# Performance work log

Measured on AMD Instinct MI355X. Metric: run time of the kernel, lower is better.

The kernel has to match this reference:

```python
import jax, jax.numpy as jnp
import numpy as np

B, L, D, H = 4, 2048, 1024, 16
HD = D // H
EPS_LN = 1e-12
EPS_Z = 1e-6


def _rope_tables(seq_len, d_model, base=10000.0):
    k_max = d_model // 2
    theta = 1.0 / (base ** (np.arange(k_max, dtype=np.float32) / k_max))
    ang = np.arange(seq_len, dtype=np.float32)[:, None] * theta[None, :]  # [L, D/2]
    return jnp.asarray(np.cos(ang)), jnp.asarray(np.sin(ang))


def _apply_rope(x, cos, sin):
    # x: [B, L, D]; complex rotation on (even, odd) pairs of last dim
    xr, xi = x[..., 0::2], x[..., 1::2]          # [B, L, D/2]
    or_ = xr * cos - xi * sin
    oi = xr * sin + xi * cos
    return jnp.stack([or_, oi], axis=-1).reshape(x.shape)


def _layernorm(x, g, b):
    mu = jnp.mean(x, axis=-1, keepdims=True)
    var = jnp.mean(jnp.square(x - mu), axis=-1, keepdims=True)
    return (x - mu) * jax.lax.rsqrt(var + EPS_LN) * g + b


def _heads(t):
    # [B, L, D] -> [B, H, L, HD]
    return t.reshape(B, L, H, HD).transpose(0, 2, 1, 3)


def _attn(x, W_qk, b_qk, conv_w, conv_b, cos, sin):
    # x: [B, L, D] (output of in_proj)
    qk = x @ W_qk + b_qk                                  # [B, L, 2D]
    q = jax.nn.elu(qk[..., :D]) + 1.0
    k = jax.nn.elu(qk[..., D:]) + 1.0
    v = x
    q_rope = _heads(_apply_rope(q, cos, sin))             # [B, H, L, HD]
    k_rope = _heads(_apply_rope(k, cos, sin))
    qh, kh, vh = _heads(q), _heads(k), _heads(v)
    # normalizer: 1 / (q . mean_L(k))
    k_mean = jnp.mean(kh, axis=2)                          # [B, H, HD]
    z = 1.0 / (jnp.einsum('bhld,bhd->bhl', qh, k_mean) + EPS_Z)  # [B, H, L]
    # kv accumulation (global, scaled by 1/L via two L^-0.5 factors)
    kv = jnp.einsum('bhld,bhle->bhde', k_rope, vh) / L     # [B, H, HD, HD]
    out = jnp.einsum('bhld,bhde->bhle', q_rope, kv) * z[..., None]  # [B,H,L,HD]
    out = out.transpose(0, 2, 1, 3).reshape(B, L, D)
    # depthwise causal conv + SiLU on v (left pad k-1=3, keep length L)
    v_t = v.transpose(0, 2, 1)                             # [B, D, L]
    conv = jax.lax.conv_general_dilated(
        v_t, conv_w, window_strides=(1,), padding=[(3, 0)],
        dimension_numbers=('NCH', 'OIH', 'NCH'), feature_group_count=D)
    conv = jax.nn.silu(conv + conv_b[:, None])             # [B, D, L]
    return out + conv.transpose(0, 2, 1)


def setup_inputs() -> dict:
    key = jax.random.key(0)
    ks = jax.random.split(key, 12)
    s = 0.02
    return {
        'x': jax.random.normal(ks[0], (B, L, D), jnp.float32),
        'ln1_g': jnp.ones((D,), jnp.float32), 'ln1_b': jnp.zeros((D,), jnp.float32),
        'ln2_g': jnp.ones((D,), jnp.float32), 'ln2_b': jnp.zeros((D,), jnp.float32),
        'W_act': jax.random.normal(ks[1], (D, D), jnp.float32) * s,
        'b_act': jnp.zeros((D,), jnp.float32),
        'W_in': jax.random.normal(ks[2], (D, D), jnp.float32) * s,
        'b_in': jnp.zeros((D,), jnp.float32),
        'W_qk': jax.random.normal(ks[3], (D, 2 * D), jnp.float32) * s,
        'b_qk': jnp.zeros((2 * D,), jnp.float32),
        'conv_w': jax.random.normal(ks[4], (D, 1, 4), jnp.float32) * 0.25,
        'conv_b': jnp.zeros((D,), jnp.float32),
        'W_out': jax.random.normal(ks[5], (D, D), jnp.float32) * s,
        'b_out': jnp.zeros((D,), jnp.float32),
        'W1': jax.random.normal(ks[6], (D, 4 * D), jnp.float32) * s,
        'b1': jnp.zeros((4 * D,), jnp.float32),
        'W2': jax.random.normal(ks[7], (4 * D, D), jnp.float32) * s,
        'b2': jnp.zeros((D,), jnp.float32),
    }


def reference(x, ln1_g, ln1_b, ln2_g, ln2_b, W_act, b_act, W_in, b_in,
              W_qk, b_qk, conv_w, conv_b, W_out, b_out, W1, b1, W2, b2):
    cos, sin = _rope_tables(L, D)
    shortcut = x
    h = _layernorm(x, ln1_g, ln1_b)
    act_res = jax.nn.silu(h @ W_act + b_act)
    h = h @ W_in + b_in
    h = _attn(h, W_qk, b_qk, conv_w, conv_b, cos, sin)
    h = (h * act_res) @ W_out + b_out
    x = shortcut + h
    m = _layernorm(x, ln2_g, ln2_b)
    m = jax.nn.gelu(m @ W1 + b1, approximate=False) @ W2 + b2
    return x + m
```

## Files before the change

### kernel.cpp

```cpp
#include <hip/hip_runtime.h>
#include <math.h>

typedef unsigned short ushort_t;
typedef __attribute__((ext_vector_type(4))) float f32x4;
typedef __attribute__((ext_vector_type(8))) __bf16 bf16x8;
typedef __attribute__((ext_vector_type(8))) unsigned short u16x8;
typedef __attribute__((ext_vector_type(4))) unsigned short u16x4;

#define DEV __device__ __forceinline__

#define CB 4
#define CL 2048
#define CD 1024
#define CM 8192

DEV float bf2f(ushort_t u) {
  unsigned int x = ((unsigned int)u) << 16;
  return __builtin_bit_cast(float, x);
}
DEV ushort_t f2bf(float f) {
  unsigned int u = __builtin_bit_cast(unsigned int, f);
  u += 0x7FFFu + ((u >> 16) & 1u);
  return (ushort_t)(u >> 16);
}
DEV void gload16(const void* g, void* l) {
  __builtin_amdgcn_global_load_lds((const __attribute__((address_space(1))) void*)g,
                                   (__attribute__((address_space(3))) void*)l, 16, 0, 0);
}
DEV bf16x8 frag64(const ushort_t* s, int row, int slog) {
  int sl = slog ^ (row & 7);
  return __builtin_bit_cast(bf16x8, *reinterpret_cast<const u16x8*>(s + row * 64 + sl * 8));
}

DEV void tr_tile(const float* __restrict__ src, ushort_t* __restrict__ dst, int R, int C, int bx,
                 int by, int t) {
  __shared__ float tile[32][33];
  int c0 = bx * 32, r0 = by * 32;
  int tx = t & 31, ty = t >> 5;
#pragma unroll
  for (int i = 0; i < 32; i += 8) tile[ty + i][tx] = src[(size_t)(r0 + ty + i) * C + c0 + tx];
  __syncthreads();
#pragma unroll
  for (int i = 0; i < 32; i += 8) dst[(size_t)(c0 + ty + i) * R + r0 + tx] = f2bf(tile[tx][ty + i]);
}

__global__ __launch_bounds__(256) void k_prep(const float* __restrict__ W_act,
                                              const float* __restrict__ W_in,
                                              const float* __restrict__ W_qk,
                                              const float* __restrict__ W_out,
                                              const float* __restrict__ W1,
                                              const float* __restrict__ W2,
                                              ushort_t* __restrict__ WabT,
                                              ushort_t* __restrict__ WqkT,
                                              ushort_t* __restrict__ WoutT,
                                              ushort_t* __restrict__ W1T,
                                              ushort_t* __restrict__ W2T,
                                              ushort_t* __restrict__ cosT,
                                              ushort_t* __restrict__ sinT) {
  int bid = blockIdx.x, t = threadIdx.x;
  if (bid < 4096) {
    int idx = bid * 256 + t;
    int l = idx >> 9, j = idx & 511;
    float theta = exp2f(-(float)j * (13.2877123795494f / 512.0f));
    float ang = (float)l * theta;
    float s, c;
    sincosf(ang, &s, &c);
    cosT[idx] = f2bf(c);
    sinT[idx] = f2bf(s);
  } else if (bid < 5120) {
    int lo = bid - 4096;
    tr_tile(W_act, WabT, 1024, 1024, lo & 31, lo >> 5, t);
  } else if (bid < 6144) {
    int lo = bid - 5120;
    tr_tile(W_in, WabT + (size_t)1024 * 1024, 1024, 1024, lo & 31, lo >> 5, t);
  } else if (bid < 8192) {
    int lo = bid - 6144;
    tr_tile(W_qk, WqkT, 1024, 2048, lo & 63, lo >> 6, t);
  } else if (bid < 9216) {
    int lo = bid - 8192;
    tr_tile(W_out, WoutT, 1024, 1024, lo & 31, lo >> 5, t);
  } else if (bid < 13312) {
    int lo = bid - 9216;
    tr_tile(W1, W1T, 1024, 4096, lo & 127, lo >> 7, t);
  } else {
    int lo = bid - 13312;
    tr_tile(W2, W2T, 4096, 1024, lo & 31, lo >> 5, t);
  }
}

__global__ __launch_bounds__(256) void k_layernorm(const float* __restrict__ x,
                                                   const float* __restrict__ g,
                                                   const float* __restrict__ b,
                                                   ushort_t* __restrict__ out) {
  int row = blockIdx.x, t = threadIdx.x;
  const float* xr = x + (size_t)row * CD;
  f32x4 v = ((const f32x4*)xr)[t];
  float s = v.x + v.y + v.z + v.w;
  float s2 = v.x * v.x + v.y * v.y + v.z * v.z + v.w * v.w;
#pragma unroll
  for (int off = 32; off >= 1; off >>= 1) {
    s += __shfl_xor(s, off);
    s2 += __shfl_xor(s2, off);
  }
  __shared__ float red[8];
  int lane = t & 63, w = t >> 6;
  if (lane == 0) { red[w] = s; red[w + 4] = s2; }
  __syncthreads();
  s = red[0] + red[1] + red[2] + red[3];
  s2 = red[4] + red[5] + red[6] + red[7];
  float mu = s * (1.0f / CD);
  float var = s2 * (1.0f / CD) - mu * mu;
  float rs = rsqrtf(var + 1e-12f);
  f32x4 gg = ((const f32x4*)g)[t];
  f32x4 bb = ((const f32x4*)b)[t];
  u16x4 o;
  o.x = f2bf((v.x - mu) * rs * gg.x + bb.x);
  o.y = f2bf((v.y - mu) * rs * gg.y + bb.y);
  o.z = f2bf((v.z - mu) * rs * gg.z + bb.z);
  o.w = f2bf((v.w - mu) * rs * gg.w + bb.w);
  ((u16x4*)(out + (size_t)row * CD))[t] = o;
}

enum { EP_AV = 0, EP_ELU1 = 1, EP_GELU = 2, EP_ADDX = 3 };

template <int EP>
__global__ __launch_bounds__(256, 4) void k_gemm(const ushort_t* __restrict__ A,
                                                 const ushort_t* __restrict__ Bt, int N, int K,
                                                 const float* __restrict__ bias,
                                                 const float* __restrict__ bias2,
                                                 const float* __restrict__ addf,
                                                 float* __restrict__ outf,
                                                 ushort_t* __restrict__ outb,
                                                 ushort_t* __restrict__ out2) {
  __shared__ __align__(16) ushort_t sA[128 * 64];
  __shared__ __align__(16) ushort_t sB[128 * 64];
  const int t = threadIdx.x;
  const int lane = t & 63;
  const int w = t >> 6;
  const int wr = w >> 1, wc = w & 1;
  const int m0 = blockIdx.y * 128, n0 = blockIdx.x * 128;

  f32x4 acc[4][4];
#pragma unroll
  for (int i = 0; i < 4; ++i)
#pragma unroll
    for (int j = 0; j < 4; ++j) acc[i][j] = f32x4{0.f, 0.f, 0.f, 0.f};

  for (int kt = 0; kt < K; kt += 64) {
#pragma unroll
    for (int i = 0; i < 4; ++i) {
      int c = t + i * 256;
      int row = c >> 3;
      int sl = (c & 7) ^ (row & 7);
      int ldsoff = (w * 64 + i * 256) * 8;
      gload16(A + (size_t)(m0 + row) * K + kt + sl * 8, sA + ldsoff);
      gload16(Bt + (size_t)(n0 + row) * K + kt + sl * 8, sB + ldsoff);
    }
    __syncthreads();
#pragma unroll
    for (int kk = 0; kk < 2; ++kk) {
      int slog = kk * 4 + (lane >> 4);
      bf16x8 af[4], bfr[4];
#pragma unroll
      for (int mi = 0; mi < 4; ++mi) af[mi] = frag64(sA, wr * 64 + mi * 16 + (lane & 15), slog);
#pragma unroll
      for (int ni = 0; ni < 4; ++ni) bfr[ni] = frag64(sB, wc * 64 + ni * 16 + (lane & 15), slog);
#pragma unroll
      for (int mi = 0; mi < 4; ++mi)
#pragma unroll
        for (int ni = 0; ni < 4; ++ni)
          acc[mi][ni] =
              __builtin_amdgcn_mfma_f32_16x16x32_bf16(af[mi], bfr[ni], acc[mi][ni], 0, 0, 0);
    }
    __syncthreads();
  }

#pragma unroll
  for (int mi = 0; mi < 4; ++mi) {
#pragma unroll
    for (int ni = 0; ni < 4; ++ni) {
      int col = n0 + wc * 64 + ni * 16 + (lane & 15);
#pragma unroll
      for (int r = 0; r < 4; ++r) {
        int row = m0 + wr * 64 + mi * 16 + (lane >> 4) * 4 + r;
        if constexpr (EP == EP_AV) {
          if (col < 1024) {
            float vv = acc[mi][ni][r] + bias[col];
            outb[(size_t)row * 1024 + col] = f2bf(vv / (1.f + expf(-vv)));
          } else {
            float vv = acc[mi][ni][r] + bias2[col - 1024];
            out2[(size_t)row * 1024 + (col - 1024)] = f2bf(vv);
          }
        } else if constexpr (EP == EP_ELU1) {
          float vv = acc[mi][ni][r] + bias[col];
          outb[(size_t)row * N + col] = f2bf(vv > 0.f ? vv + 1.f : expf(vv));
        } else if constexpr (EP == EP_GELU) {
          float vv = acc[mi][ni][r] + bias[col];
          outb[(size_t)row * N + col] = f2bf(0.5f * vv * (1.f + erff(vv * 0.70710678118654752f)));
        } else {
          size_t idx = (size_t)row * N + col;
          outf[idx] = addf[idx] + acc[mi][ni][r] + bias[col];
        }
      }
    }
  }
}

__global__ __launch_bounds__(256) void k_attn_reduce(const ushort_t* __restrict__ qk,
                                                     const ushort_t* __restrict__ vbf,
                                                     const ushort_t* __restrict__ cosT,
                                                     const ushort_t* __restrict__ sinT,
                                                     float* __restrict__ kvpart,
                                                     float* __restrict__ kmpart) {
  int bh = blockIdx.x >> 2, ls = blockIdx.x & 3;
  int b = bh >> 4, h = bh & 15;
  int t = threadIdx.x, lane = t & 63, w = t >> 6;

  __shared__ float kst[64][68];
  __shared__ __align__(16) ushort_t krT[64 * 64];
  __shared__ __align__(16) ushort_t vT[64 * 64];
  __shared__ float cst[64][32];
  __shared__ float snt[64][32];
  __shared__ float kmp[4][64];

  float kmacc = 0.f;
  f32x4 acc[4];
#pragma unroll
  for (int i = 0; i < 4; ++i) acc[i] = f32x4{0.f, 0.f, 0.f, 0.f};

  for (int c = ls * 8; c < ls * 8 + 8; ++c) {
    int l0 = c * 64;
    for (int idx = t; idx < 4096; idx += 256) {
      int l = idx >> 6, d = idx & 63;
      size_t grow = (size_t)(b * CL + l0 + l);
      float kvv = bf2f(qk[grow * 2048 + 1024 + h * 64 + d]);
      kst[l][d] = kvv;
      kmacc += kvv;
      ushort_t vv = vbf[grow * CD + h * 64 + d];
      int sl = (l >> 3) ^ (d & 7);
      vT[d * 64 + sl * 8 + (l & 7)] = vv;
    }
    for (int idx = t; idx < 2048; idx += 256) {
      int l = idx >> 5, j = idx & 31;
      size_t p = (size_t)(l0 + l) * 512 + h * 32 + j;
      cst[l][j] = bf2f(cosT[p]);
      snt[l][j] = bf2f(sinT[p]);
    }
    __syncthreads();
    for (int idx = t; idx < 4096; idx += 256) {
      int l = idx >> 6, d = idx & 63, j = d >> 1;
      float cc = cst[l][j], sn = snt[l][j];
      float kr = (d & 1) ? (kst[l][d - 1] * sn + kst[l][d] * cc)
                         : (kst[l][d] * cc - kst[l][d + 1] * sn);
      int sl = (l >> 3) ^ (d & 7);
      krT[d * 64 + sl * 8 + (l & 7)] = f2bf(kr);
    }
    __syncthreads();
#pragma unroll
    for (int kk = 0; kk < 2; ++kk) {
      int slog = kk * 4 + (lane >> 4);
      bf16x8 a = frag64(vT, w * 16 + (lane & 15), slog);
#pragma unroll
      for (int ni = 0; ni < 4; ++ni) {
        bf16x8 bb = frag64(krT, ni * 16 + (lane & 15), slog);
        acc[ni] = __builtin_amdgcn_mfma_f32_16x16x32_bf16(a, bb, acc[ni], 0, 0, 0);
      }
    }
    __syncthreads();
  }
  float* kp = kvpart + ((size_t)(bh * 4 + ls)) * 4096;
#pragma unroll
  for (int ni = 0; ni < 4; ++ni) {
    int d = ni * 16 + (lane & 15);
#pragma unroll
    for (int r = 0; r < 4; ++r) {
      int e = w * 16 + (lane >> 4) * 4 + r;
      kp[e * 64 + d] = acc[ni][r];
    }
  }
  kmp[t >> 6][t & 63] = kmacc;
  __syncthreads();
  if (t < 64) kmpart[(bh * 4 + ls) * 64 + t] = kmp[0][t] + kmp[1][t] + kmp[2][t] + kmp[3][t];
}

__global__ void k_kv_reduce(const float* __restrict__ kvpart, const float* __restrict__ kmpart,
                            ushort_t* __restrict__ kvT, float* __restrict__ kmean) {
  int gid = blockIdx.x * 256 + threadIdx.x;
  int bh = gid >> 12;
  int r = gid & 4095;
  float s = 0.f;
#pragma unroll
  for (int ls = 0; ls < 4; ++ls) s += kvpart[((size_t)(bh * 4 + ls)) * 4096 + r];
  kvT[gid] = f2bf(s);
  if (gid < 64 * 64) {
    int bh2 = gid >> 6, d = gid & 63;
    float m = 0.f;
#pragma unroll
    for (int ls = 0; ls < 4; ++ls) m += kmpart[(bh2 * 4 + ls) * 64 + d];
    kmean[gid] = m;
  }
}

__global__ __launch_bounds__(256) void k_attn_out(
    const ushort_t* __restrict__ qk, const ushort_t* __restrict__ kvT,
    const float* __restrict__ kmean, const ushort_t* __restrict__ cosT,
    const ushort_t* __restrict__ sinT, const ushort_t* __restrict__ vbf,
    const ushort_t* __restrict__ act, const float* __restrict__ convw,
    const float* __restrict__ convb, ushort_t* __restrict__ A4) {
  int bid = blockIdx.x;
  int bh = bid >> 5, lt = bid & 31;
  int b = bh >> 4, h = bh & 15;
  int l0 = lt * 64;
  int t = threadIdx.x, lane = t & 63, w = t >> 6;

  __shared__ float qst[64][68];
  __shared__ __align__(16) ushort_t qrT[64 * 64];
  __shared__ __align__(16) ushort_t kvs[64 * 64];
  __shared__ float cst[64][32];
  __shared__ float snt[64][32];
  __shared__ float kms[64];
  __shared__ float zrow[64];

  if (t < 64) kms[t] = kmean[bh * 64 + t];
  for (int idx = t; idx < 4096; idx += 256) {
    int l = idx >> 6, d = idx & 63;
    qst[l][d] = bf2f(qk[(size_t)(b * CL + l0 + l) * 2048 + h * 64 + d]);
    ushort_t kvv = kvT[(size_t)bh * 4096 + idx];
    int e = idx >> 6, dd = idx & 63;
    int sl = (dd >> 3) ^ (e & 7);
    kvs[e * 64 + sl * 8 + (dd & 7)] = kvv;
  }
  for (int idx = t; idx < 2048; idx += 256) {
    int l = idx >> 5, j = idx & 31;
    size_t p = (size_t)(l0 + l) * 512 + h * 32 + j;
    cst[l][j] = bf2f(cosT[p]);
    snt[l][j] = bf2f(sinT[p]);
  }
  __syncthreads();
  for (int idx = t; idx < 4096; idx += 256) {
    int l = idx >> 6, d = idx & 63, j = d >> 1;
    float cc = cst[l][j], sn = snt[l][j];
    float qr = (d & 1) ? (qst[l][d - 1] * sn + qst[l][d] * cc)
                       : (qst[l][d] * cc - qst[l][d + 1] * sn);
    int sl = (d >> 3) ^ (l & 7);
    qrT[l * 64 + sl * 8 + (d & 7)] = f2bf(qr);
  }
  if (t < 64) {
    float dot = 0.f;
#pragma unroll
    for (int d = 0; d < 64; ++d) dot += qst[t][d] * kms[d];
    zrow[t] = 1.0f / (dot * (1.0f / (float)CL) + 1e-6f);
  }
  __syncthreads();
  f32x4 acc[4];
#pragma unroll
  for (int i = 0; i < 4; ++i) acc[i] = f32x4{0.f, 0.f, 0.f, 0.f};
#pragma unroll
  for (int kk = 0; kk < 2; ++kk) {
    int slog = kk * 4 + (lane >> 4);
    bf16x8 a = frag64(qrT, w * 16 + (lane & 15), slog);
#pragma unroll
    for (int ni = 0; ni < 4; ++ni) {
      bf16x8 bb = frag64(kvs, ni * 16 + (lane & 15), slog);
      acc[ni] = __builtin_amdgcn_mfma_f32_16x16x32_bf16(a, bb, acc[ni], 0, 0, 0);
    }
  }
#pragma unroll
  for (int ni = 0; ni < 4; ++ni) {
    int e = ni * 16 + (lane & 15);
    int dcol = h * 64 + e;
#pragma unroll
    for (int r = 0; r < 4; ++r) {
      int l = w * 16 + (lane >> 4) * 4 + r;
      int lg = l0 + l;
      size_t row = (size_t)(b * CL + lg);
      float val = acc[ni][r] * zrow[l] * (1.0f / (float)CL);
      float cv = convb[dcol];
#pragma unroll
      for (int tt = 0; tt < 4; ++tt) {
        if (lg - 3 + tt >= 0) cv += bf2f(vbf[(row - 3 + tt) * CD + dcol]) * convw[dcol * 4 + tt];
      }
      cv = cv / (1.f + expf(-cv));
      float a4 = (val + cv) * bf2f(act[row * CD + dcol]);
      A4[row * CD + dcol] = f2bf(a4);
    }
  }
}

extern "C" void kernel_launch(void* const* d_in, const int* in_sizes, int n_in, void* d_out,
                              int out_size, void* d_ws, size_t ws_size, hipStream_t stream) {
  const float* x = (const float*)d_in[0];
  const float* ln1_g = (const float*)d_in[1];
  const float* ln1_b = (const float*)d_in[2];
  const float* ln2_g = (const float*)d_in[3];
  const float* ln2_b = (const float*)d_in[4];
  const float* W_act = (const float*)d_in[5];
  const float* b_act = (const float*)d_in[6];
  const float* W_in = (const float*)d_in[7];
  const float* b_in = (const float*)d_in[8];
  const float* W_qk = (const float*)d_in[9];
  const float* b_qk = (const float*)d_in[10];
  const float* conv_w = (const float*)d_in[11];
  const float* conv_b = (const float*)d_in[12];
  const float* W_out = (const float*)d_in[13];
  const float* b_out = (const float*)d_in[14];
  const float* W1 = (const float*)d_in[15];
  const float* b1 = (const float*)d_in[16];
  const float* W2 = (const float*)d_in[17];
  const float* b2 = (const float*)d_in[18];
  float* out = (float*)d_out;

  char* w = (char*)d_ws;
  const size_t MB = 1024 * 1024;
  ushort_t* cosT = (ushort_t*)(w + 0 * MB);
  ushort_t* sinT = (ushort_t*)(w + 2 * MB);
  ushort_t* WabT = (ushort_t*)(w + 4 * MB);
  ushort_t* WqkT = (ushort_t*)(w + 8 * MB);
  ushort_t* WoutT = (ushort_t*)(w + 12 * MB);
  ushort_t* kvTb = (ushort_t*)(w + 14 * MB);
  float* kmean = (float*)(w + 14 * MB + 512 * 1024);
  float* kmpart = (float*)(w + 14 * MB + 640 * 1024);
  ushort_t* mln = (ushort_t*)(w + 0 * MB);
  ushort_t* W1T = (ushort_t*)(w + 16 * MB);
  ushort_t* W2T = (ushort_t*)(w + 24 * MB);
  ushort_t* hln = (ushort_t*)(w + 32 * MB);
  ushort_t* qkb = (ushort_t*)(w + 48 * MB);
  ushort_t* actb = (ushort_t*)(w + 80 * MB);
  ushort_t* Gb = (ushort_t*)(w + 32 * MB);
  ushort_t* vb = (ushort_t*)(w + 96 * MB);
  ushort_t* A4 = (ushort_t*)(w + 112 * MB);
  float* kvpart = (float*)(w + 112 * MB);
  float* x2 = (float*)(w + 128 * MB);

  (void)in_sizes; (void)n_in; (void)out_size; (void)ws_size;

  k_prep<<<17408, 256, 0, stream>>>(W_act, W_in, W_qk, W_out, W1, W2, WabT, WqkT, WoutT, W1T, W2T,
                                    cosT, sinT);
  k_layernorm<<<CM, 256, 0, stream>>>(x, ln1_g, ln1_b, hln);
  k_gemm<EP_AV><<<dim3(16, 64), 256, 0, stream>>>(hln, WabT, 2048, 1024, b_act, b_in, nullptr,
                                                  nullptr, actb, vb);
  k_gemm<EP_ELU1><<<dim3(16, 64), 256, 0, stream>>>(vb, WqkT, 2048, 1024, b_qk, nullptr, nullptr,
                                                    nullptr, qkb, nullptr);
  k_attn_reduce<<<256, 256, 0, stream>>>(qkb, vb, cosT, sinT, kvpart, kmpart);
  k_kv_reduce<<<1024, 256, 0, stream>>>(kvpart, kmpart, kvTb, kmean);
  k_attn_out<<<2048, 256, 0, stream>>>(qkb, kvTb, kmean, cosT, sinT, vb, actb, conv_w, conv_b, A4);
  k_gemm<EP_ADDX><<<dim3(8, 64), 256, 0, stream>>>(A4, WoutT, 1024, 1024, b_out, nullptr, x, x2,
                                                   nullptr, nullptr);
  k_layernorm<<<CM, 256, 0, stream>>>(x2, ln2_g, ln2_b, mln);
  k_gemm<EP_GELU><<<dim3(32, 64), 256, 0, stream>>>(mln, W1T, 4096, 1024, b1, nullptr, nullptr,
                                                    nullptr, Gb, nullptr);
  k_gemm<EP_ADDX><<<dim3(8, 64), 256, 0, stream>>>(Gb, W2T, 1024, 4096, b2, nullptr, x2, out,
                                                   nullptr, nullptr);
}
```

Measured before the change: 470.7 us.

## Split-K the N=1024 GEMMs, fuse residual add into LayerNorm, remap block IDs

```diff
diff --git a/kernel.cpp b/kernel.cpp
--- a/kernel.cpp
+++ b/kernel.cpp
@@ -121,14 +121,64 @@
   ((u16x4*)(out + (size_t)row * CD))[t] = o;
 }
 
-enum { EP_AV = 0, EP_ELU1 = 1, EP_GELU = 2, EP_ADDX = 3 };
+__global__ __launch_bounds__(256) void k_addln(const float* __restrict__ x,
+                                               const float* __restrict__ bo,
+                                               const float* __restrict__ P,
+                                               const float* __restrict__ g,
+                                               const float* __restrict__ b,
+                                               float* __restrict__ x2,
+                                               ushort_t* __restrict__ mln) {
+  int row = blockIdx.x, t = threadIdx.x;
+  size_t base = (size_t)row * CD;
+  f32x4 v = ((const f32x4*)(x + base))[t];
+  v += ((const f32x4*)(P + base))[t];
+  v += ((const f32x4*)(P + (size_t)8388608 + base))[t];
+  v += ((const f32x4*)bo)[t];
+  ((f32x4*)(x2 + base))[t] = v;
+  float s = v.x + v.y + v.z + v.w;
+  float s2 = v.x * v.x + v.y * v.y + v.z * v.z + v.w * v.w;
+#pragma unroll
+  for (int off = 32; off >= 1; off >>= 1) {
+    s += __shfl_xor(s, off);
+    s2 += __shfl_xor(s2, off);
+  }
+  __shared__ float red[8];
+  int lane = t & 63, w = t >> 6;
+  if (lane == 0) { red[w] = s; red[w + 4] = s2; }
+  __syncthreads();
+  s = red[0] + red[1] + red[2] + red[3];
+  s2 = red[4] + red[5] + red[6] + red[7];
+  float mu = s * (1.0f / CD);
+  float var = s2 * (1.0f / CD) - mu * mu;
+  float rs = rsqrtf(var + 1e-12f);
+  f32x4 gg = ((const f32x4*)g)[t];
+  f32x4 bb = ((const f32x4*)b)[t];
+  u16x4 o;
+  o.x = f2bf((v.x - mu) * rs * gg.x + bb.x);
+  o.y = f2bf((v.y - mu) * rs * gg.y + bb.y);
+  o.z = f2bf((v.z - mu) * rs * gg.z + bb.z);
+  o.w = f2bf((v.w - mu) * rs * gg.w + bb.w);
+  ((u16x4*)(mln + base))[t] = o;
+}
+
+__global__ void k_final(const float* __restrict__ x2, const float* __restrict__ b2,
+                        const float* __restrict__ P, float* __restrict__ out) {
+  size_t i = (size_t)blockIdx.x * 256 + threadIdx.x;
+  f32x4 v = ((const f32x4*)x2)[i];
+  v += ((const f32x4*)P)[i];
+  v += ((const f32x4*)(P + 8388608))[i];
+  v += ((const f32x4*)b2)[(int)(i & 255)];
+  ((f32x4*)out)[i] = v;
+}
+
+enum { EP_AV = 0, EP_ELU1 = 1, EP_GELU = 2, EP_KS = 3 };
 
 template <int EP>
 __global__ __launch_bounds__(256, 4) void k_gemm(const ushort_t* __restrict__ A,
-                                                 const ushort_t* __restrict__ Bt, int N, int K,
+                                                 const ushort_t* __restrict__ Bt, int N, int lda,
+                                                 int ldb, int Klen, int nbx, int nks,
                                                  const float* __restrict__ bias,
                                                  const float* __restrict__ bias2,
-                                                 const float* __restrict__ addf,
                                                  float* __restrict__ outf,
                                                  ushort_t* __restrict__ outb,
                                                  ushort_t* __restrict__ out2) {
@@ -138,7 +188,17 @@
   const int lane = t & 63;
   const int w = t >> 6;
   const int wr = w >> 1, wc = w & 1;
-  const int m0 = blockIdx.y * 128, n0 = blockIdx.x * 128;
+  const int lr = lane & 15, lq = lane >> 4;
+
+  int bid = blockIdx.x;
+  int q = gridDim.x >> 3;
+  int wg = (bid & 7) * q + (bid >> 3);
+  int by = wg / (nbx * nks);
+  int rem = wg - by * (nbx * nks);
+  int bx = rem / nks;
+  int ks = rem - bx * nks;
+  const int m0 = by * 128, n0 = bx * 128;
+  const int koff = ks * Klen;
 
   f32x4 acc[4][4];
 #pragma unroll
@@ -146,25 +206,25 @@
 #pragma unroll
     for (int j = 0; j < 4; ++j) acc[i][j] = f32x4{0.f, 0.f, 0.f, 0.f};
 
-  for (int kt = 0; kt < K; kt += 64) {
+  for (int kt = 0; kt < Klen; kt += 64) {
 #pragma unroll
     for (int i = 0; i < 4; ++i) {
       int c = t + i * 256;
       int row = c >> 3;
       int sl = (c & 7) ^ (row & 7);
       int ldsoff = (w * 64 + i * 256) * 8;
-      gload16(A + (size_t)(m0 + row) * K + kt + sl * 8, sA + ldsoff);
-      gload16(Bt + (size_t)(n0 + row) * K + kt + sl * 8, sB + ldsoff);
+      gload16(A + (size_t)(m0 + row) * lda + koff + kt + sl * 8, sA + ldsoff);
+      gload16(Bt + (size_t)(n0 + row) * ldb + koff + kt + sl * 8, sB + ldsoff);
     }
     __syncthreads();
 #pragma unroll
     for (int kk = 0; kk < 2; ++kk) {
-      int slog = kk * 4 + (lane >> 4);
+      int slog = kk * 4 + lq;
       bf16x8 af[4], bfr[4];
 #pragma unroll
-      for (int mi = 0; mi < 4; ++mi) af[mi] = frag64(sA, wr * 64 + mi * 16 + (lane & 15), slog);
-#pragma unroll
-      for (int ni = 0; ni < 4; ++ni) bfr[ni] = frag64(sB, wc * 64 + ni * 16 + (lane & 15), slog);
+      for (int mi = 0; mi < 4; ++mi) af[mi] = frag64(sA, wr * 64 + mi * 16 + lr, slog);
+#pragma unroll
+      for (int ni = 0; ni < 4; ++ni) bfr[ni] = frag64(sB, wc * 64 + ni * 16 + lr, slog);
 #pragma unroll
       for (int mi = 0; mi < 4; ++mi)
 #pragma unroll
@@ -179,10 +239,10 @@
   for (int mi = 0; mi < 4; ++mi) {
 #pragma unroll
     for (int ni = 0; ni < 4; ++ni) {
-      int col = n0 + wc * 64 + ni * 16 + (lane & 15);
+      int col = n0 + wc * 64 + ni * 16 + lr;
 #pragma unroll
       for (int r = 0; r < 4; ++r) {
-        int row = m0 + wr * 64 + mi * 16 + (lane >> 4) * 4 + r;
+        int row = m0 + wr * 64 + mi * 16 + lq * 4 + r;
         if constexpr (EP == EP_AV) {
           if (col < 1024) {
             float vv = acc[mi][ni][r] + bias[col];
@@ -198,8 +258,7 @@
           float vv = acc[mi][ni][r] + bias[col];
           outb[(size_t)row * N + col] = f2bf(0.5f * vv * (1.f + erff(vv * 0.70710678118654752f)));
         } else {
-          size_t idx = (size_t)row * N + col;
-          outf[idx] = addf[idx] + acc[mi][ni][r] + bias[col];
+          outf[(size_t)ks * 8388608 + (size_t)row * N + col] = acc[mi][ni][r];
         }
       }
     }
@@ -430,25 +489,27 @@
   ushort_t* vb = (ushort_t*)(w + 96 * MB);
   ushort_t* A4 = (ushort_t*)(w + 112 * MB);
   float* kvpart = (float*)(w + 112 * MB);
-  float* x2 = (float*)(w + 128 * MB);
+  float* x2 = (float*)(w + 96 * MB);
+  float* PP = (float*)(w + 128 * MB);
 
   (void)in_sizes; (void)n_in; (void)out_size; (void)ws_size;
 
   k_prep<<<17408, 256, 0, stream>>>(W_act, W_in, W_qk, W_out, W1, W2, WabT, WqkT, WoutT, W1T, W2T,
                                     cosT, sinT);
   k_layernorm<<<CM, 256, 0, stream>>>(x, ln1_g, ln1_b, hln);
-  k_gemm<EP_AV><<<dim3(16, 64), 256, 0, stream>>>(hln, WabT, 2048, 1024, b_act, b_in, nullptr,
-                                                  nullptr, actb, vb);
-  k_gemm<EP_ELU1><<<dim3(16, 64), 256, 0, stream>>>(vb, WqkT, 2048, 1024, b_qk, nullptr, nullptr,
-                                                    nullptr, qkb, nullptr);
+  k_gemm<EP_AV><<<1024, 256, 0, stream>>>(hln, WabT, 2048, 1024, 1024, 1024, 16, 1, b_act, b_in,
+                                          nullptr, actb, vb);
+  k_gemm<EP_ELU1><<<1024, 256, 0, stream>>>(vb, WqkT, 2048, 1024, 1024, 1024, 16, 1, b_qk, nullptr,
+                                            nullptr, qkb, nullptr);
   k_attn_reduce<<<256, 256, 0, stream>>>(qkb, vb, cosT, sinT, kvpart, kmpart);
   k_kv_reduce<<<1024, 256, 0, stream>>>(kvpart, kmpart, kvTb, kmean);
   k_attn_out<<<2048, 256, 0, stream>>>(qkb, kvTb, kmean, cosT, sinT, vb, actb, conv_w, conv_b, A4);
-  k_gemm<EP_ADDX><<<dim3(8, 64), 256, 0, stream>>>(A4, WoutT, 1024, 1024, b_out, nullptr, x, x2,
-                                                   nullptr, nullptr);
-  k_layernorm<<<CM, 256, 0, stream>>>(x2, ln2_g, ln2_b, mln);
-  k_gemm<EP_GELU><<<dim3(32, 64), 256, 0, stream>>>(mln, W1T, 4096, 1024, b1, nullptr, nullptr,
-                                                    nullptr, Gb, nullptr);
-  k_gemm<EP_ADDX><<<dim3(8, 64), 256, 0, stream>>>(Gb, W2T, 1024, 4096, b2, nullptr, x2, out,
-                                                   nullptr, nullptr);
-}
+  k_gemm<EP_KS><<<1024, 256, 0, stream>>>(A4, WoutT, 1024, 1024, 1024, 512, 8, 2, nullptr, nullptr,
+                                          PP, nullptr, nullptr);
+  k_addln<<<CM, 256, 0, stream>>>(x, b_out, PP, ln2_g, ln2_b, x2, mln);
+  k_gemm<EP_GELU><<<2048, 256, 0, stream>>>(mln, W1T, 4096, 1024, 1024, 1024, 32, 1, b1, nullptr,
+                                            nullptr, Gb, nullptr);
+  k_gemm<EP_KS><<<1024, 256, 0, stream>>>(Gb, W2T, 1024, 4096, 4096, 2048, 8, 2, nullptr, nullptr,
+                                          PP, nullptr, nullptr);
+  k_final<<<8192, 256, 0, stream>>>(x2, b2, PP, out);
+}
```

After: 513.5 us. 9.1% more time.

## Add pipelined 256x256 GEMM kernel for FFN up-projection with tanh GELU

Applied to the files above, without the earlier changes.

```diff
diff --git a/kernel.cpp b/kernel.cpp
--- a/kernel.cpp
+++ b/kernel.cpp
@@ -30,6 +30,12 @@
 DEV bf16x8 frag64(const ushort_t* s, int row, int slog) {
   int sl = slog ^ (row & 7);
   return __builtin_bit_cast(bf16x8, *reinterpret_cast<const u16x8*>(s + row * 64 + sl * 8));
+}
+DEV float gelu_f(float x) {
+  float u = 0.7978845608f * (x + 0.044715f * x * x * x);
+  float e = __expf(2.0f * u);
+  float th = 1.0f - 2.0f / (e + 1.0f);
+  return 0.5f * x * (1.0f + th);
 }
 
 DEV void tr_tile(const float* __restrict__ src, ushort_t* __restrict__ dst, int R, int C, int bx,
@@ -64,7 +70,7 @@
     float theta = exp2f(-(float)j * (13.2877123795494f / 512.0f));
     float ang = (float)l * theta;
     float s, c;
-    sincosf(ang, &s, &c);
+    __sincosf(ang, &s, &c);
     cosT[idx] = f2bf(c);
     sinT[idx] = f2bf(s);
   } else if (bid < 5120) {
@@ -121,7 +127,7 @@
   ((u16x4*)(out + (size_t)row * CD))[t] = o;
 }
 
-enum { EP_AV = 0, EP_ELU1 = 1, EP_GELU = 2, EP_ADDX = 3 };
+enum { EP_AV = 0, EP_ELU1 = 1, EP_ADDX = 3 };
 
 template <int EP>
 __global__ __launch_bounds__(256, 4) void k_gemm(const ushort_t* __restrict__ A,
@@ -138,6 +144,7 @@
   const int lane = t & 63;
   const int w = t >> 6;
   const int wr = w >> 1, wc = w & 1;
+  const int lr = lane & 15, lq = lane >> 4;
   const int m0 = blockIdx.y * 128, n0 = blockIdx.x * 128;
 
   f32x4 acc[4][4];
@@ -159,12 +166,12 @@
     __syncthreads();
 #pragma unroll
     for (int kk = 0; kk < 2; ++kk) {
-      int slog = kk * 4 + (lane >> 4);
+      int slog = kk * 4 + lq;
       bf16x8 af[4], bfr[4];
 #pragma unroll
-      for (int mi = 0; mi < 4; ++mi) af[mi] = frag64(sA, wr * 64 + mi * 16 + (lane & 15), slog);
-#pragma unroll
-      for (int ni = 0; ni < 4; ++ni) bfr[ni] = frag64(sB, wc * 64 + ni * 16 + (lane & 15), slog);
+      for (int mi = 0; mi < 4; ++mi) af[mi] = frag64(sA, wr * 64 + mi * 16 + lr, slog);
+#pragma unroll
+      for (int ni = 0; ni < 4; ++ni) bfr[ni] = frag64(sB, wc * 64 + ni * 16 + lr, slog);
 #pragma unroll
       for (int mi = 0; mi < 4; ++mi)
 #pragma unroll
@@ -179,28 +186,143 @@
   for (int mi = 0; mi < 4; ++mi) {
 #pragma unroll
     for (int ni = 0; ni < 4; ++ni) {
-      int col = n0 + wc * 64 + ni * 16 + (lane & 15);
+      int col = n0 + wc * 64 + ni * 16 + lr;
 #pragma unroll
       for (int r = 0; r < 4; ++r) {
-        int row = m0 + wr * 64 + mi * 16 + (lane >> 4) * 4 + r;
+        int row = m0 + wr * 64 + mi * 16 + lq * 4 + r;
         if constexpr (EP == EP_AV) {
           if (col < 1024) {
             float vv = acc[mi][ni][r] + bias[col];
-            outb[(size_t)row * 1024 + col] = f2bf(vv / (1.f + expf(-vv)));
+            outb[(size_t)row * 1024 + col] = f2bf(vv / (1.f + __expf(-vv)));
           } else {
             float vv = acc[mi][ni][r] + bias2[col - 1024];
             out2[(size_t)row * 1024 + (col - 1024)] = f2bf(vv);
           }
         } else if constexpr (EP == EP_ELU1) {
           float vv = acc[mi][ni][r] + bias[col];
-          outb[(size_t)row * N + col] = f2bf(vv > 0.f ? vv + 1.f : expf(vv));
-        } else if constexpr (EP == EP_GELU) {
-          float vv = acc[mi][ni][r] + bias[col];
-          outb[(size_t)row * N + col] = f2bf(0.5f * vv * (1.f + erff(vv * 0.70710678118654752f)));
+          outb[(size_t)row * N + col] = f2bf(vv > 0.f ? vv + 1.f : __expf(vv));
         } else {
           size_t idx = (size_t)row * N + col;
           outf[idx] = addf[idx] + acc[mi][ni][r] + bias[col];
         }
+      }
+    }
+  }
+}
+
+#define STGA8(h_, kt_, b_)                                                              \
+  {                                                                                     \
+    gload16(pA0 + (size_t)(h_)*131072 + (kt_), smem + (b_)*32768 + (h_)*8192 + dof0);   \
+    gload16(pA1 + (size_t)(h_)*131072 + (kt_), smem + (b_)*32768 + (h_)*8192 + dof1);   \
+  }
+#define STGB8(h_, kt_, b_)                                                                  \
+  {                                                                                         \
+    gload16(pB0 + (size_t)(h_)*131072 + (kt_), smem + (b_)*32768 + 16384 + (h_)*8192 + dof0); \
+    gload16(pB1 + (size_t)(h_)*131072 + (kt_), smem + (b_)*32768 + 16384 + (h_)*8192 + dof1); \
+  }
+#define PHASE8(mh_, nh_, RA_, BF_, RB_)                                                     \
+  {                                                                                         \
+    if (RA_) {                                                                              \
+      _Pragma("unroll") for (int mi = 0; mi < 4; ++mi)                                      \
+          _Pragma("unroll") for (int kk = 0; kk < 2; ++kk)                                  \
+              af[mi][kk] = frag64(sA, wr * 128 + (mh_)*64 + mi * 16 + lr, kk * 4 + lq);     \
+    }                                                                                       \
+    if (RB_) {                                                                              \
+      _Pragma("unroll") for (int ni = 0; ni < 2; ++ni)                                      \
+          _Pragma("unroll") for (int kk = 0; kk < 2; ++kk)                                  \
+              BF_[ni][kk] = frag64(sB, wc * 64 + (nh_)*32 + ni * 16 + lr, kk * 4 + lq);     \
+    }                                                                                       \
+    __builtin_amdgcn_s_barrier();                                                           \
+    asm volatile("s_waitcnt lgkmcnt(0)" ::: "memory");                                      \
+    __builtin_amdgcn_sched_barrier(0);                                                      \
+    __builtin_amdgcn_s_setprio(1);                                                          \
+    _Pragma("unroll") for (int kk = 0; kk < 2; ++kk)                                        \
+        _Pragma("unroll") for (int mi = 0; mi < 4; ++mi)                                    \
+            _Pragma("unroll") for (int ni = 0; ni < 2; ++ni)                                \
+                acc[(mh_)*4 + mi][(nh_)*2 + ni] = __builtin_amdgcn_mfma_f32_16x16x32_bf16(  \
+                    af[mi][kk], BF_[ni][kk], acc[(mh_)*4 + mi][(nh_)*2 + ni], 0, 0, 0);     \
+    __builtin_amdgcn_s_setprio(0);                                                          \
+    __builtin_amdgcn_sched_barrier(0);                                                      \
+    __builtin_amdgcn_s_barrier();                                                           \
+  }
+
+__global__ __launch_bounds__(512, 1) void k_gemm8(const ushort_t* __restrict__ A,
+                                                  const ushort_t* __restrict__ Bt, int N, int lda,
+                                                  int ldb, int Klen, int nbx,
+                                                  const float* __restrict__ bias,
+                                                  ushort_t* __restrict__ outb) {
+  __shared__ __align__(16) ushort_t smem[2 * 32768];
+  const int t = threadIdx.x;
+  const int lane = t & 63, w = t >> 6;
+  const int wr = w >> 2, wc = w & 3;
+  const int lr = lane & 15, lq = lane >> 4;
+
+  int bid = blockIdx.x;
+  int by = bid / nbx, bx = bid - by * nbx;
+  const int m0 = by << 8, n0 = bx << 8;
+
+  int c0_ = t, r0_ = c0_ >> 3, s0_ = (c0_ & 7) ^ (r0_ & 7);
+  int c1_ = t + 512, r1_ = c1_ >> 3, s1_ = (c1_ & 7) ^ (r1_ & 7);
+  const ushort_t* pA0 = A + (size_t)(m0 + r0_) * lda + s0_ * 8;
+  const ushort_t* pA1 = A + (size_t)(m0 + r1_) * lda + s1_ * 8;
+  const ushort_t* pB0 = Bt + (size_t)(n0 + r0_) * ldb + s0_ * 8;
+  const ushort_t* pB1 = Bt + (size_t)(n0 + r1_) * ldb + s1_ * 8;
+  const int dof0 = (w * 64) * 8;
+  const int dof1 = (w * 64 + 512) * 8;
+
+  f32x4 acc[8][4];
+#pragma unroll
+  for (int i = 0; i < 8; ++i)
+#pragma unroll
+    for (int j = 0; j < 4; ++j) acc[i][j] = f32x4{0.f, 0.f, 0.f, 0.f};
+
+  const int NT = Klen >> 6;
+  STGA8(0, 0, 0);
+  STGA8(1, 0, 0);
+  STGB8(0, 0, 0);
+  STGB8(1, 0, 0);
+  STGA8(0, 64, 1);
+  asm volatile("s_waitcnt vmcnt(2)" ::: "memory");
+  __builtin_amdgcn_s_barrier();
+  __builtin_amdgcn_sched_barrier(0);
+
+  bf16x8 af[4][2], bf0[2][2], bf1[2][2];
+  for (int tt = 0; tt < NT; ++tt) {
+    const int buf = tt & 1, nbuf = buf ^ 1;
+    const int ktn = (tt + 1) << 6;
+    const ushort_t* sA = smem + buf * 32768;
+    const ushort_t* sB = sA + 16384;
+    const bool more = (tt + 1 < NT);
+    if (more) STGA8(1, ktn, nbuf);
+    PHASE8(0, 0, 1, bf0, 1)
+    if (more) STGB8(0, ktn, nbuf);
+    PHASE8(0, 1, 0, bf1, 1)
+    if (more) STGB8(1, ktn, nbuf);
+    PHASE8(1, 1, 1, bf1, 0)
+    PHASE8(1, 0, 0, bf0, 0)
+    if (more) {
+      if (tt + 2 < NT) {
+        STGA8(0, (tt + 2) << 6, buf);
+        asm volatile("s_waitcnt vmcnt(2)" ::: "memory");
+      } else {
+        asm volatile("s_waitcnt vmcnt(0)" ::: "memory");
+      }
+      __builtin_amdgcn_s_barrier();
+      __builtin_amdgcn_sched_barrier(0);
+    }
+  }
+
+#pragma unroll
+  for (int mi = 0; mi < 8; ++mi) {
+#pragma unroll
+    for (int ni = 0; ni < 4; ++ni) {
+      int col = n0 + wc * 64 + ni * 16 + lr;
+      float bc = bias[col];
+#pragma unroll
+      for (int r = 0; r < 4; ++r) {
+        int row = m0 + wr * 128 + mi * 16 + lq * 4 + r;
+        float vv = acc[mi][ni][r] + bc;
+        outb[(size_t)row * N + col] = f2bf(gelu_f(vv));
       }
     }
   }
@@ -380,7 +502,7 @@
       for (int tt = 0; tt < 4; ++tt) {
         if (lg - 3 + tt >= 0) cv += bf2f(vbf[(row - 3 + tt) * CD + dcol]) * convw[dcol * 4 + tt];
       }
-      cv = cv / (1.f + expf(-cv));
+      cv = cv / (1.f + __expf(-cv));
       float a4 = (val + cv) * bf2f(act[row * CD + dcol]);
       A4[row * CD + dcol] = f2bf(a4);
     }
@@ -447,8 +569,7 @@
   k_gemm<EP_ADDX><<<dim3(8, 64), 256, 0, stream>>>(A4, WoutT, 1024, 1024, b_out, nullptr, x, x2,
                                                    nullptr, nullptr);
   k_layernorm<<<CM, 256, 0, stream>>>(x2, ln2_g, ln2_b, mln);
-  k_gemm<EP_GELU><<<dim3(32, 64), 256, 0, stream>>>(mln, W1T, 4096, 1024, b1, nullptr, nullptr,
-                                                    nullptr, Gb, nullptr);
+  k_gemm8<<<512, 512, 0, stream>>>(mln, W1T, 4096, 1024, 1024, 1024, 16, b1, Gb);
   k_gemm<EP_ADDX><<<dim3(8, 64), 256, 0, stream>>>(Gb, W2T, 1024, 4096, b2, nullptr, x2, out,
                                                    nullptr, nullptr);
 }
```

Result: faster. 448.6 us (-4.7%).
